# Performance work log

Hardware: AMD Instinct MI355X
Metric: run time of the kernel (lower is better)

The kernel has to match this reference:

```python
import jax, jax.numpy as jnp
import numpy as np

B, N, D, K, H, L = 4, 20000, 64, 256, 4, 2
F = 4 * D
DH = D // H
SCALE = DH ** -0.5
EPS = 1e-5


def _layernorm(x, g, b):
    m = jnp.mean(x, axis=-1, keepdims=True)
    v = jnp.mean(jnp.square(x - m), axis=-1, keepdims=True)
    return (x - m) / jnp.sqrt(v + EPS) * g + b


def setup_inputs() -> dict:
    key = jax.random.key(0)
    ks = jax.random.split(key, 12)
    s = 0.02
    return {
        'expr': jax.random.normal(ks[0], (B, N), jnp.float32),
        'emb': jax.random.normal(ks[1], (N, D), jnp.float32),
        'Wq': jax.random.normal(ks[2], (L, D, D), jnp.float32) * s,
        'Wk': jax.random.normal(ks[3], (L, D, D), jnp.float32) * s,
        'Wv': jax.random.normal(ks[4], (L, D, D), jnp.float32) * s,
        'projK': jax.random.normal(ks[5], (L, N, K), jnp.float32) * s,
        'projV': jax.random.normal(ks[6], (L, N, K), jnp.float32) * s,
        'Wo': jax.random.normal(ks[7], (L, D, D), jnp.float32) * s,
        'bo': jnp.zeros((L, D), jnp.float32),
        'g1': jnp.ones((L, D), jnp.float32),
        'be1': jnp.zeros((L, D), jnp.float32),
        'W1': jax.random.normal(ks[8], (L, D, F), jnp.float32) * s,
        'bf1': jnp.zeros((L, F), jnp.float32),
        'W2': jax.random.normal(ks[9], (L, F, D), jnp.float32) * s,
        'bf2': jnp.zeros((L, D), jnp.float32),
        'g2': jnp.ones((L, D), jnp.float32),
        'be2': jnp.zeros((L, D), jnp.float32),
    }


def _forward(expr, emb, Wq, Wk, Wv, projK, projV, Wo, bo, g1, be1, W1, bf1, W2, bf2, g2, be2):
    # gene_ids = arange(N) for every batch row -> embedding lookup is just the table
    x = emb[None, :, :] * expr[:, :, None]  # [B, N, D]
    for i in range(L):
        b = x.shape[0]
        # Linformer self-attention
        q = jnp.einsum('bnd,de->bne', x, Wq[i])                 # [B, N, D]
        k_low = jnp.einsum('bnd,nk->bkd', x, projK[i])          # [B, K, D]
        v_low = jnp.einsum('bnd,nk->bkd', x, projV[i])          # [B, K, D]
        k = jnp.einsum('bkd,de->bke', k_low, Wk[i])             # [B, K, D]
        v = jnp.einsum('bkd,de->bke', v_low, Wv[i])             # [B, K, D]
        qh = q.reshape(b, N, H, DH).transpose(0, 2, 1, 3)       # [B, H, N, DH]
        kh = k.reshape(b, K, H, DH).transpose(0, 2, 1, 3)       # [B, H, K, DH]
        vh = v.reshape(b, K, H, DH).transpose(0, 2, 1, 3)       # [B, H, K, DH]
        dots = jnp.einsum('bhnd,bhkd->bhnk', qh, kh) * SCALE    # [B, H, N, K]
        attn = jax.nn.softmax(dots, axis=-1)
        o = jnp.einsum('bhnk,bhkd->bhnd', attn, vh)             # [B, H, N, DH]
        o = o.transpose(0, 2, 1, 3).reshape(b, N, D)
        o = jnp.einsum('bnd,de->bne', o, Wo[i]) + bo[i]
        x = _layernorm(o + x, g1[i], be1[i])
        # FFN (exact GELU, matching torch nn.GELU default)
        h = jax.nn.gelu(jnp.einsum('bnd,df->bnf', x, W1[i]) + bf1[i], approximate=False)
        f = jnp.einsum('bnf,fd->bnd', h, W2[i]) + bf2[i]
        x = _layernorm(f + x, g2[i], be2[i])
    return x


def reference(expr, emb, Wq, Wk, Wv, projK, projV, Wo, bo, g1, be1, W1, bf1, W2, bf2, g2, be2):
    return _forward(expr, emb, Wq, Wk, Wv, projK, projV, Wo, bo, g1, be1, W1, bf1, W2, bf2, g2, be2)
```

## Files before the change

### kernel.cpp

```cpp
#include <hip/hip_runtime.h>

using u16 = unsigned short;
typedef __bf16 bf16x8 __attribute__((ext_vector_type(8)));
typedef u16    u16x8  __attribute__((ext_vector_type(8)));
typedef u16    u16x4  __attribute__((ext_vector_type(4)));
typedef float  f32x4  __attribute__((ext_vector_type(4)));
typedef float  f32x16 __attribute__((ext_vector_type(16)));
typedef unsigned uint4v __attribute__((ext_vector_type(4)));

#define DEV static __device__ __forceinline__

constexpr int NB = 4;
constexpr int NN = 20000;
constexpr int DD = 64;
constexpr int KK = 256;
constexpr int ROWS = NB * NN;

DEV float b2f(u16 u) { union { unsigned i; float f; } c; c.i = ((unsigned)u) << 16; return c.f; }
DEV u16 f2b(float f) {
  union { float f; unsigned i; } c; c.f = f;
  unsigned i = c.i + 0x7FFFu + ((c.i >> 16) & 1u);
  return (u16)(i >> 16);
}
DEV bf16x8 ldb8(const u16* p) { return *reinterpret_cast<const bf16x8*>(p); }
DEV f32x16 mfma32(bf16x8 a, bf16x8 b, f32x16 c) { return __builtin_amdgcn_mfma_f32_32x32x16_bf16(a, b, c, 0, 0, 0); }

DEV unsigned cvtpk(float lo, float hi) {
  unsigned r;
  asm("v_cvt_pk_bf16_f32 %0, %1, %2" : "=v"(r) : "v"(lo), "v"(hi));
  return r;
}
DEV void swap32(unsigned& a, unsigned& b) {
  auto r = __builtin_amdgcn_permlane32_swap((int)a, (int)b, false, false);
  a = (unsigned)r[0]; b = (unsigned)r[1];
}

__global__ __launch_bounds__(256) void k_pre(
    const float* __restrict__ expr, const float* __restrict__ emb,
    const float* __restrict__ Wq, const float* __restrict__ Wo,
    const float* __restrict__ W1, const float* __restrict__ W2,
    const float* __restrict__ projK, const float* __restrict__ projV,
    u16* __restrict__ wb, u16* __restrict__ pKT, u16* __restrict__ pVT,
    u16* __restrict__ xb, u16* __restrict__ ones) {
  __shared__ float lds[64][65];
  int bid = blockIdx.x;
  int t = threadIdx.x;
  if (bid < 5008) {
    int nt = bid % 313, q = bid / 313, kt = q & 3, z = q >> 2;
    int layer = z & 1, pv = z >> 1;
    const float* src = (pv ? projV : projK) + (size_t)layer * NN * KK;
    u16* dst = (pv ? pVT : pKT) + (size_t)layer * KK * NN;
    int n0 = nt * 64, k0 = kt * 64;
    int r = t >> 4, c4 = (t & 15) * 4;
#pragma unroll
    for (int i = 0; i < 4; ++i) {
      int rr = r + i * 16;
      float4 v = make_float4(0.f, 0.f, 0.f, 0.f);
      if (n0 + rr < NN) v = *reinterpret_cast<const float4*>(&src[(size_t)(n0 + rr) * KK + k0 + c4]);
      lds[c4 + 0][rr] = v.x; lds[c4 + 1][rr] = v.y; lds[c4 + 2][rr] = v.z; lds[c4 + 3][rr] = v.w;
    }
    __syncthreads();
    int kr = t >> 3, nb = (t & 7) * 8;
#pragma unroll
    for (int p = 0; p < 2; ++p) {
      int k = kr + p * 32;
      if (n0 + nb < NN) {
        u16x8 o;
#pragma unroll
        for (int j = 0; j < 8; ++j) o[j] = f2b(lds[k][nb + j]);
        *reinterpret_cast<u16x8*>(&dst[(size_t)(k0 + k) * NN + n0 + nb]) = o;
      }
    }
  } else if (bid < 7508) {
    int idx8 = ((bid - 5008) * 256 + t) * 8;
    int b = idx8 / (NN * DD);
    int rem = idx8 - b * (NN * DD);
    int n = rem >> 6, d = rem & 63;
    float4 e0 = *reinterpret_cast<const float4*>(&emb[(n << 6) + d]);
    float4 e1 = *reinterpret_cast<const float4*>(&emb[(n << 6) + d + 4]);
    float s = expr[b * NN + n];
    u16x8 o;
    o[0] = f2b(e0.x * s); o[1] = f2b(e0.y * s); o[2] = f2b(e0.z * s); o[3] = f2b(e0.w * s);
    o[4] = f2b(e1.x * s); o[5] = f2b(e1.y * s); o[6] = f2b(e1.z * s); o[7] = f2b(e1.w * s);
    *reinterpret_cast<u16x8*>(&xb[idx8]) = o;
  } else if (bid < 7572) {
    int b2 = bid - 7508;
    int bx = b2 & 7, m = (b2 >> 3) & 3, l = b2 >> 5;
    const float* src; u16* dst; int Dout, S, CT;
    if (m == 0)      { src = Wq + l * 4096;  dst = wb + l * 4096;          Dout = 64;  S = 4;  CT = 2; }
    else if (m == 1) { src = Wo + l * 4096;  dst = wb + 8192 + l * 4096;   Dout = 64;  S = 4;  CT = 2; }
    else if (m == 2) { src = W1 + l * 16384; dst = wb + 16384 + l * 16384; Dout = 256; S = 4;  CT = 8; }
    else             { src = W2 + l * 16384; dst = wb + 49152 + l * 16384; Dout = 64;  S = 16; CT = 2; }
    int slot = bx * 256 + t;
    if (slot >= S * CT * 64) return;
    int s = slot / (CT * 64), rem = slot % (CT * 64);
    int ct = rem >> 6, lane = rem & 63;
    int hi = lane >> 5, lo = lane & 31;
    u16x8 o;
#pragma unroll
    for (int j = 0; j < 8; ++j) o[j] = f2b(src[(s * 16 + hi * 8 + j) * Dout + ct * 32 + lo]);
    *reinterpret_cast<u16x8*>(&dst[slot * 8]) = o;
  } else {
    ones[t] = 0x3F80;
  }
}

__global__ __launch_bounds__(256) void k_qxt(
    const u16* __restrict__ x, const u16* __restrict__ WB,
    u16* __restrict__ qb, u16* __restrict__ xT) {
  __shared__ u16 ldsx[64][70];
  int bid = blockIdx.x;
  int t = threadIdx.x;
  if (bid < 625) {
    int w = t >> 6, lane = t & 63;
    int lo = lane & 31, hi = lane >> 5;
    int unit = bid * 4 + w;
    bf16x8 wf[4][2];
#pragma unroll
    for (int s = 0; s < 4; ++s)
#pragma unroll
      for (int ct = 0; ct < 2; ++ct) wf[s][ct] = ldb8(&WB[((s * 2 + ct) * 64 + lane) * 8]);
    f32x16 acc[2] = {};
    int r0 = unit * 32;
#pragma unroll
    for (int s = 0; s < 4; ++s) {
      bf16x8 a = ldb8(&x[(size_t)(r0 + lo) * 64 + s * 16 + hi * 8]);
      acc[0] = mfma32(a, wf[s][0], acc[0]);
      acc[1] = mfma32(a, wf[s][1], acc[1]);
    }
#pragma unroll
    for (int reg = 0; reg < 16; ++reg) {
      int row = r0 + (reg & 3) + 8 * (reg >> 2) + 4 * hi;
      qb[(size_t)row * 64 + lo] = f2b(acc[0][reg]);
      qb[(size_t)row * 64 + 32 + lo] = f2b(acc[1][reg]);
    }
  } else {
    int v = bid - 625;
    int nt = v % 313, b = v / 313;
    int n0 = nt * 64;
    int r = t >> 4, c4 = (t & 15) * 4;
    const u16* xbp = x + (size_t)b * NN * 64;
#pragma unroll
    for (int i = 0; i < 4; ++i) {
      int rr = r + i * 16;
      u16x4 vv = {};
      if (n0 + rr < NN) vv = *reinterpret_cast<const u16x4*>(&xbp[(size_t)(n0 + rr) * 64 + c4]);
      ldsx[c4 + 0][rr] = vv[0]; ldsx[c4 + 1][rr] = vv[1];
      ldsx[c4 + 2][rr] = vv[2]; ldsx[c4 + 3][rr] = vv[3];
    }
    __syncthreads();
    int dr = t >> 3, nb = (t & 7) * 8;
    u16* xo = xT + (size_t)b * 64 * NN;
#pragma unroll
    for (int p = 0; p < 2; ++p) {
      int d = dr + p * 32;
      if (n0 + nb < NN) {
        u16x8 o;
#pragma unroll
        for (int j = 0; j < 8; ++j) o[j] = ldsx[d][nb + j];
        *reinterpret_cast<u16x8*>(&xo[(size_t)d * NN + n0 + nb]) = o;
      }
    }
  }
}

__global__ __launch_bounds__(256) void k_proj(
    const u16* __restrict__ xT, const u16* __restrict__ pKT_l, const u16* __restrict__ pVT_l,
    float* __restrict__ part) {
  int c = blockIdx.x, b = blockIdx.y, proj = blockIdx.z;
  const u16* P = proj ? pVT_l : pKT_l;
  int t = threadIdx.x, w = t >> 6, lane = t & 63;
  int lo = lane & 31, hi = lane >> 5;
  int d0 = (w & 1) * 32;
  int kbase = (w >> 1) * 128;
  int n0 = c * 512;
  int rem = NN - n0;
  int steps = (rem < 512 ? rem : 512) >> 4;
  const u16* xr = xT + ((size_t)b * 64 + d0 + lo) * NN;
  f32x16 acc[4] = {};
  int s = 0;
  for (; s + 4 <= steps; s += 4) {
    bf16x8 a[4]; bf16x8 bv[4][4];
#pragma unroll
    for (int u = 0; u < 4; ++u) {
      int nb = n0 + (s + u) * 16 + hi * 8;
      a[u] = ldb8(&xr[nb]);
#pragma unroll
      for (int g = 0; g < 4; ++g) bv[u][g] = ldb8(&P[(size_t)(kbase + g * 32 + lo) * NN + nb]);
    }
#pragma unroll
    for (int u = 0; u < 4; ++u)
#pragma unroll
      for (int g = 0; g < 4; ++g) acc[g] = mfma32(a[u], bv[u][g], acc[g]);
  }
  for (; s < steps; ++s) {
    int nb = n0 + s * 16 + hi * 8;
    bf16x8 a = ldb8(&xr[nb]);
#pragma unroll
    for (int g = 0; g < 4; ++g) acc[g] = mfma32(a, ldb8(&P[(size_t)(kbase + g * 32 + lo) * NN + nb]), acc[g]);
  }
  float* dst = part + ((size_t)(proj * NB + b) * 40 + c) * (64 * 256);
#pragma unroll
  for (int g = 0; g < 4; ++g)
#pragma unroll
    for (int r = 0; r < 16; ++r) {
      int d = d0 + (r & 3) + 8 * (r >> 2) + 4 * hi;
      dst[d * 256 + kbase + g * 32 + lo] = acc[g][r];
    }
}

__global__ __launch_bounds__(256) void k_p2(
    const float* __restrict__ part, const float* __restrict__ Wk_l, const float* __restrict__ Wv_l,
    u16* __restrict__ kbuf, u16* __restrict__ vT) {
  int ks = blockIdx.x, b = blockIdx.y, proj = blockIdx.z;
  int k0 = ks * 8;
  const float* W = proj ? Wv_l : Wk_l;
  __shared__ float low[64][8];
  int t = threadIdx.x;
  const float* src = part + (size_t)(proj * NB + b) * 40 * (64 * 256);
#pragma unroll
  for (int i = 0; i < 2; ++i) {
    int idx = i * 256 + t;
    int e = idx >> 3, k = idx & 7;
    float s = 0.f;
    for (int cc = 0; cc < 40; ++cc) s += src[(size_t)cc * (64 * 256) + e * 256 + k0 + k];
    low[e][k] = s;
  }
  __syncthreads();
#pragma unroll
  for (int i = 0; i < 2; ++i) {
    int idx = i * 256 + t;
    int d = idx & 63, kk = idx >> 6;
    float a = 0.f;
#pragma unroll
    for (int e = 0; e < 64; ++e) a += low[e][kk] * W[e * 64 + d];
    if (proj == 0) {
      kbuf[((size_t)b * KK + k0 + kk) * 64 + d] = f2b(a * 0.3606737602222409f);
    } else {
      vT[((size_t)b * 64 + d) * KK + k0 + kk] = f2b(a);
    }
  }
}

__global__ __launch_bounds__(256) void k_attn(
    const u16* __restrict__ q, const u16* __restrict__ kbuf, const u16* __restrict__ vT,
    const u16* __restrict__ ones, u16* __restrict__ ao) {
  int t = threadIdx.x, h = t >> 6, lane = t & 63;
  int lo = lane & 31, hi = lane >> 5;
  int b = blockIdx.y;
  int n0 = blockIdx.x * 32;
  const u16* qb = q + (size_t)b * NN * 64;
  const u16* kb = kbuf + (size_t)b * KK * 64 + h * 16;
  const u16* vsrc = (lo < 16)
      ? vT + (size_t)b * 64 * KK + (size_t)(h * 16 + lo) * KK
      : ones;
  bf16x8 qf = ldb8(&qb[(size_t)(n0 + lo) * 64 + h * 16 + hi * 8]);
  f32x16 acc = {};
#pragma unroll
  for (int kt = 0; kt < 8; ++kt) {
    bf16x8 kf = ldb8(&kb[(size_t)(kt * 32 + lo) * 64 + hi * 8]);
    f32x16 z = {};
    f32x16 s = mfma32(kf, qf, z);
    float e[16];
#pragma unroll
    for (int r = 0; r < 16; ++r) e[r] = __builtin_amdgcn_exp2f(s[r]);
#pragma unroll
    for (int c = 0; c < 2; ++c) {
      unsigned Aw = cvtpk(e[c * 8 + 0], e[c * 8 + 1]);
      unsigned Bw = cvtpk(e[c * 8 + 2], e[c * 8 + 3]);
      unsigned Cw = cvtpk(e[c * 8 + 4], e[c * 8 + 5]);
      unsigned Dw = cvtpk(e[c * 8 + 6], e[c * 8 + 7]);
      swap32(Aw, Cw);
      swap32(Bw, Dw);
      uint4v pk; pk.x = Aw; pk.y = Bw; pk.z = Cw; pk.w = Dw;
      bf16x8 af = ldb8(&vsrc[kt * 32 + c * 16 + hi * 8]);
      acc = mfma32(af, __builtin_bit_cast(bf16x8, pk), acc);
    }
  }
  float inv = __builtin_amdgcn_rcpf(acc[8]);
  float o[8];
#pragma unroll
  for (int r = 0; r < 8; ++r) o[r] = acc[r] * inv;
  unsigned Aw = cvtpk(o[0], o[1]);
  unsigned Bw = cvtpk(o[2], o[3]);
  unsigned Cw = cvtpk(o[4], o[5]);
  unsigned Dw = cvtpk(o[6], o[7]);
  swap32(Aw, Cw);
  swap32(Bw, Dw);
  uint4v st; st.x = Aw; st.y = Bw; st.z = Cw; st.w = Dw;
  *reinterpret_cast<uint4v*>(&ao[(size_t)b * NN * 64 + (size_t)(n0 + lo) * 64 + h * 16 + hi * 8]) = st;
}

__global__ __launch_bounds__(256) void k_oln(
    const u16* __restrict__ A, const u16* __restrict__ WB,
    const float* __restrict__ bias, const u16* __restrict__ res,
    const float* __restrict__ g, const float* __restrict__ be, u16* __restrict__ out) {
  int t = threadIdx.x, w = t >> 6, lane = t & 63;
  int lo = lane & 31, hi = lane >> 5;
  int unit = blockIdx.x * 4 + w;
  bf16x8 wf[4][2];
#pragma unroll
  for (int s = 0; s < 4; ++s)
#pragma unroll
    for (int ct = 0; ct < 2; ++ct) wf[s][ct] = ldb8(&WB[((s * 2 + ct) * 64 + lane) * 8]);
  float bia[2], gg[2], bb[2];
#pragma unroll
  for (int ct = 0; ct < 2; ++ct) {
    bia[ct] = bias[ct * 32 + lo];
    gg[ct] = g[ct * 32 + lo];
    bb[ct] = be[ct * 32 + lo];
  }
  f32x16 acc[2] = {};
  int r0 = unit * 32;
#pragma unroll
  for (int s = 0; s < 4; ++s) {
    bf16x8 a = ldb8(&A[(size_t)(r0 + lo) * 64 + s * 16 + hi * 8]);
    acc[0] = mfma32(a, wf[s][0], acc[0]);
    acc[1] = mfma32(a, wf[s][1], acc[1]);
  }
#pragma unroll
  for (int reg = 0; reg < 16; ++reg) {
    int row = r0 + (reg & 3) + 8 * (reg >> 2) + 4 * hi;
    float a0 = acc[0][reg] + bia[0] + b2f(res[(size_t)row * 64 + lo]);
    float a1 = acc[1][reg] + bia[1] + b2f(res[(size_t)row * 64 + 32 + lo]);
    float su = a0 + a1, sq = a0 * a0 + a1 * a1;
#pragma unroll
    for (int m = 1; m <= 16; m <<= 1) { su += __shfl_xor(su, m); sq += __shfl_xor(sq, m); }
    float mean = su * (1.f / 64.f);
    float var = sq * (1.f / 64.f) - mean * mean;
    float rstd = rsqrtf(var + 1e-5f);
    out[(size_t)row * 64 + lo] = f2b((a0 - mean) * rstd * gg[0] + bb[0]);
    out[(size_t)row * 64 + 32 + lo] = f2b((a1 - mean) * rstd * gg[1] + bb[1]);
  }
}

__global__ __launch_bounds__(256, 2) void k_gemm_64_256(
    const u16* __restrict__ A, const u16* __restrict__ WB,
    const float* __restrict__ bias, u16* __restrict__ out) {
  int t = threadIdx.x, w = t >> 6, lane = t & 63;
  int lo = lane & 31, hi = lane >> 5;
  int colg = w & 1;
  int unit = blockIdx.x * 2 + (w >> 1);
  bf16x8 wf[4][4];
  float bia[4];
#pragma unroll
  for (int s = 0; s < 4; ++s)
#pragma unroll
    for (int ct = 0; ct < 4; ++ct) wf[s][ct] = ldb8(&WB[((s * 8 + colg * 4 + ct) * 64 + lane) * 8]);
#pragma unroll
  for (int ct = 0; ct < 4; ++ct) bia[ct] = bias[colg * 128 + ct * 32 + lo];
  f32x16 acc[4] = {};
  int r0 = unit * 32;
#pragma unroll
  for (int s = 0; s < 4; ++s) {
    bf16x8 a = ldb8(&A[(size_t)(r0 + lo) * 64 + s * 16 + hi * 8]);
#pragma unroll
    for (int ct = 0; ct < 4; ++ct) acc[ct] = mfma32(a, wf[s][ct], acc[ct]);
  }
#pragma unroll
  for (int ct = 0; ct < 4; ++ct) {
#pragma unroll
    for (int reg = 0; reg < 16; ++reg) {
      int row = r0 + (reg & 3) + 8 * (reg >> 2) + 4 * hi;
      float x = acc[ct][reg] + bia[ct];
      float gel = 0.5f * x * (1.f + erff(x * 0.7071067811865475f));
      out[(size_t)row * 256 + colg * 128 + ct * 32 + lo] = f2b(gel);
    }
  }
}

__global__ __launch_bounds__(256) void k_gemm_256_64(
    const u16* __restrict__ A, const u16* __restrict__ WB,
    const float* __restrict__ bias, const u16* __restrict__ res,
    const float* __restrict__ g, const float* __restrict__ be,
    u16* __restrict__ outb, float* __restrict__ outf) {
  int t = threadIdx.x, w = t >> 6, lane = t & 63;
  int lo = lane & 31, hi = lane >> 5;
  int unit = blockIdx.x * 4 + w;
  float bia[2], gg[2], bb[2];
#pragma unroll
  for (int ct = 0; ct < 2; ++ct) {
    bia[ct] = bias[ct * 32 + lo];
    gg[ct] = g[ct * 32 + lo];
    bb[ct] = be[ct * 32 + lo];
  }
  f32x16 acc[2] = {};
  int r0 = unit * 32;
#pragma unroll
  for (int s = 0; s < 16; ++s) {
    bf16x8 w0 = ldb8(&WB[((s * 2 + 0) * 64 + lane) * 8]);
    bf16x8 w1 = ldb8(&WB[((s * 2 + 1) * 64 + lane) * 8]);
    bf16x8 a = ldb8(&A[(size_t)(r0 + lo) * 256 + s * 16 + hi * 8]);
    acc[0] = mfma32(a, w0, acc[0]);
    acc[1] = mfma32(a, w1, acc[1]);
  }
#pragma unroll
  for (int reg = 0; reg < 16; ++reg) {
    int row = r0 + (reg & 3) + 8 * (reg >> 2) + 4 * hi;
    float a0 = acc[0][reg] + bia[0] + b2f(res[(size_t)row * 64 + lo]);
    float a1 = acc[1][reg] + bia[1] + b2f(res[(size_t)row * 64 + 32 + lo]);
    float su = a0 + a1, sq = a0 * a0 + a1 * a1;
#pragma unroll
    for (int m = 1; m <= 16; m <<= 1) { su += __shfl_xor(su, m); sq += __shfl_xor(sq, m); }
    float mean = su * (1.f / 64.f);
    float var = sq * (1.f / 64.f) - mean * mean;
    float rstd = rsqrtf(var + 1e-5f);
    float o0 = (a0 - mean) * rstd * gg[0] + bb[0];
    float o1 = (a1 - mean) * rstd * gg[1] + bb[1];
    if (outb) {
      outb[(size_t)row * 64 + lo] = f2b(o0);
      outb[(size_t)row * 64 + 32 + lo] = f2b(o1);
    }
    if (outf) {
      outf[(size_t)row * 64 + lo] = o0;
      outf[(size_t)row * 64 + 32 + lo] = o1;
    }
  }
}

extern "C" void kernel_launch(void* const* d_in, const int* in_sizes, int n_in,
                              void* d_out, int out_size, void* d_ws, size_t ws_size,
                              hipStream_t stream) {
  const float* expr = (const float*)d_in[0];
  const float* emb  = (const float*)d_in[1];
  const float* Wq   = (const float*)d_in[2];
  const float* Wk   = (const float*)d_in[3];
  const float* Wv   = (const float*)d_in[4];
  const float* projK = (const float*)d_in[5];
  const float* projV = (const float*)d_in[6];
  const float* Wo   = (const float*)d_in[7];
  const float* bo   = (const float*)d_in[8];
  const float* g1   = (const float*)d_in[9];
  const float* be1  = (const float*)d_in[10];
  const float* W1   = (const float*)d_in[11];
  const float* bf1  = (const float*)d_in[12];
  const float* W2   = (const float*)d_in[13];
  const float* bf2  = (const float*)d_in[14];
  const float* g2   = (const float*)d_in[15];
  const float* be2  = (const float*)d_in[16];
  float* out = (float*)d_out;
  char* ws = (char*)d_ws;

  u16* xb0 = (u16*)(ws + 0);
  u16* xb1 = (u16*)(ws + 10240000);
  u16* xb2 = (u16*)(ws + 20480000);
  u16* qb  = (u16*)(ws + 30720000);
  u16* aob = (u16*)(ws + 40960000);
  u16* hb  = (u16*)(ws + 51200000);
  float* part = (float*)(ws + 51200000);
  u16* pKT = (u16*)(ws + 92160000);
  u16* pVT = (u16*)(ws + 112640000);
  u16* xTb = (u16*)(ws + 133120000);
  u16* kB  = (u16*)(ws + 143360000);
  u16* vTB = (u16*)(ws + 143491072);
  u16* wb  = (u16*)(ws + 143622144);
  u16* ones = (u16*)(ws + 143785984);

  k_pre<<<7573, 256, 0, stream>>>(expr, emb, Wq, Wo, W1, W2, projK, projV,
                                  wb, pKT, pVT, xb0, ones);

  const u16* xin = xb0;
  for (int l = 0; l < 2; ++l) {
    const u16* wbq = wb + l * 4096;
    const u16* wbo = wb + 8192 + l * 4096;
    const u16* wb1 = wb + 16384 + l * 16384;
    const u16* wb2 = wb + 49152 + l * 16384;
    k_qxt<<<1877, 256, 0, stream>>>(xin, wbq, qb, xTb);
    k_proj<<<dim3(40, NB, 2), 256, 0, stream>>>(xTb, pKT + (size_t)l * KK * NN, pVT + (size_t)l * KK * NN, part);
    k_p2<<<dim3(32, NB, 2), 256, 0, stream>>>(part, Wk + l * 4096, Wv + l * 4096, kB, vTB);
    k_attn<<<dim3(625, NB), 256, 0, stream>>>(qb, kB, vTB, ones, aob);
    k_oln<<<625, 256, 0, stream>>>(aob, wbo, bo + l * 64, xin, g1 + l * 64, be1 + l * 64, xb1);
    k_gemm_64_256<<<1250, 256, 0, stream>>>(xb1, wb1, bf1 + l * 256, hb);
    k_gemm_256_64<<<625, 256, 0, stream>>>(hb, wb2, bf2 + l * 64, xb1,
                                           g2 + l * 64, be2 + l * 64,
                                           l == 0 ? xb2 : nullptr, l == 1 ? out : nullptr);
    xin = xb2;
  }
}
```

Measured before the change: 421.9 us.

## Fuse FFN up/down GEMMs with GELU in registers; widen projection transpose tiles

Merges the two FFN kernels into one. The GELU hidden activations stay in registers: they are repacked with permlane32 swaps into MFMA operand layout and fed straight into the second GEMM, with the residual add and layernorm folded into the epilogue. This removes the round-trip of the B×N×256 bf16 hidden tensor through global memory and one launch per layer. The preprocessing kernel also uses 128-row transpose tiles for the projection matrices, and the W1/W2 weight packing is changed to the transposed-operand layout the fused kernel expects. In exchange, each wave runs the whole FFN serially with more live registers, which may lower occupancy.

Result: faster. 405.1 us (-4.0%).

```diff
diff --git a/kernel.cpp b/kernel.cpp
--- a/kernel.cpp
+++ b/kernel.cpp
@@ -42,28 +42,35 @@
     const float* __restrict__ projK, const float* __restrict__ projV,
     u16* __restrict__ wb, u16* __restrict__ pKT, u16* __restrict__ pVT,
     u16* __restrict__ xb, u16* __restrict__ ones) {
-  __shared__ float lds[64][65];
+  __shared__ float lds[64][130];
   int bid = blockIdx.x;
   int t = threadIdx.x;
-  if (bid < 5008) {
-    int nt = bid % 313, q = bid / 313, kt = q & 3, z = q >> 2;
+  if (bid < 2512) {
+    int nt = bid % 157, q = bid / 157, kt = q & 3, z = q >> 2;
     int layer = z & 1, pv = z >> 1;
     const float* src = (pv ? projV : projK) + (size_t)layer * NN * KK;
     u16* dst = (pv ? pVT : pKT) + (size_t)layer * KK * NN;
-    int n0 = nt * 64, k0 = kt * 64;
-    int r = t >> 4, c4 = (t & 15) * 4;
-#pragma unroll
-    for (int i = 0; i < 4; ++i) {
-      int rr = r + i * 16;
-      float4 v = make_float4(0.f, 0.f, 0.f, 0.f);
-      if (n0 + rr < NN) v = *reinterpret_cast<const float4*>(&src[(size_t)(n0 + rr) * KK + k0 + c4]);
-      lds[c4 + 0][rr] = v.x; lds[c4 + 1][rr] = v.y; lds[c4 + 2][rr] = v.z; lds[c4 + 3][rr] = v.w;
+    int n0 = nt * 128, k0 = kt * 64;
+    int nr = t >> 1, kh = (t & 1) * 32;
+    float4 vv[8];
+    bool okr = (n0 + nr < NN);
+#pragma unroll
+    for (int q8 = 0; q8 < 8; ++q8) {
+      vv[q8] = make_float4(0.f, 0.f, 0.f, 0.f);
+      if (okr) vv[q8] = *reinterpret_cast<const float4*>(&src[(size_t)(n0 + nr) * KK + k0 + kh + q8 * 4]);
+    }
+#pragma unroll
+    for (int q8 = 0; q8 < 8; ++q8) {
+      lds[kh + q8 * 4 + 0][nr] = vv[q8].x;
+      lds[kh + q8 * 4 + 1][nr] = vv[q8].y;
+      lds[kh + q8 * 4 + 2][nr] = vv[q8].z;
+      lds[kh + q8 * 4 + 3][nr] = vv[q8].w;
     }
     __syncthreads();
-    int kr = t >> 3, nb = (t & 7) * 8;
-#pragma unroll
-    for (int p = 0; p < 2; ++p) {
-      int k = kr + p * 32;
+    int nb = (t & 15) * 8, kr = t >> 4;
+#pragma unroll
+    for (int p = 0; p < 4; ++p) {
+      int k = kr + p * 16;
       if (n0 + nb < NN) {
         u16x8 o;
 #pragma unroll
@@ -71,8 +78,8 @@
         *reinterpret_cast<u16x8*>(&dst[(size_t)(k0 + k) * NN + n0 + nb]) = o;
       }
     }
-  } else if (bid < 7508) {
-    int idx8 = ((bid - 5008) * 256 + t) * 8;
+  } else if (bid < 5012) {
+    int idx8 = ((bid - 2512) * 256 + t) * 8;
     int b = idx8 / (NN * DD);
     int rem = idx8 - b * (NN * DD);
     int n = rem >> 6, d = rem & 63;
@@ -83,23 +90,38 @@
     o[0] = f2b(e0.x * s); o[1] = f2b(e0.y * s); o[2] = f2b(e0.z * s); o[3] = f2b(e0.w * s);
     o[4] = f2b(e1.x * s); o[5] = f2b(e1.y * s); o[6] = f2b(e1.z * s); o[7] = f2b(e1.w * s);
     *reinterpret_cast<u16x8*>(&xb[idx8]) = o;
-  } else if (bid < 7572) {
-    int b2 = bid - 7508;
+  } else if (bid < 5076) {
+    int b2 = bid - 5012;
     int bx = b2 & 7, m = (b2 >> 3) & 3, l = b2 >> 5;
-    const float* src; u16* dst; int Dout, S, CT;
-    if (m == 0)      { src = Wq + l * 4096;  dst = wb + l * 4096;          Dout = 64;  S = 4;  CT = 2; }
-    else if (m == 1) { src = Wo + l * 4096;  dst = wb + 8192 + l * 4096;   Dout = 64;  S = 4;  CT = 2; }
-    else if (m == 2) { src = W1 + l * 16384; dst = wb + 16384 + l * 16384; Dout = 256; S = 4;  CT = 8; }
-    else             { src = W2 + l * 16384; dst = wb + 49152 + l * 16384; Dout = 64;  S = 16; CT = 2; }
     int slot = bx * 256 + t;
-    if (slot >= S * CT * 64) return;
-    int s = slot / (CT * 64), rem = slot % (CT * 64);
-    int ct = rem >> 6, lane = rem & 63;
-    int hi = lane >> 5, lo = lane & 31;
     u16x8 o;
-#pragma unroll
-    for (int j = 0; j < 8; ++j) o[j] = f2b(src[(s * 16 + hi * 8 + j) * Dout + ct * 32 + lo]);
-    *reinterpret_cast<u16x8*>(&dst[slot * 8]) = o;
+    if (m <= 1) {
+      if (slot >= 512) return;
+      int s = slot >> 7, rem = slot & 127;
+      int ct = rem >> 6, lane = rem & 63;
+      int hi = lane >> 5, lo = lane & 31;
+      const float* src = (m == 0 ? Wq : Wo) + l * 4096;
+      u16* dst = wb + (m == 0 ? 0 : 8192) + l * 4096;
+#pragma unroll
+      for (int j = 0; j < 8; ++j) o[j] = f2b(src[(s * 16 + hi * 8 + j) * 64 + ct * 32 + lo]);
+      *reinterpret_cast<u16x8*>(&dst[slot * 8]) = o;
+    } else if (m == 2) {
+      int ftile = slot >> 8, s = (slot >> 6) & 3, lane = slot & 63;
+      int hi = lane >> 5, lo = lane & 31;
+      const float* src = W1 + l * 16384;
+      u16* dst = wb + 16384 + l * 16384;
+#pragma unroll
+      for (int j = 0; j < 8; ++j) o[j] = f2b(src[(s * 16 + hi * 8 + j) * 256 + ftile * 32 + lo]);
+      *reinterpret_cast<u16x8*>(&dst[slot * 8]) = o;
+    } else {
+      int dtile = slot >> 10, s2 = (slot >> 6) & 15, lane = slot & 63;
+      int hi = lane >> 5, lo = lane & 31;
+      const float* src = W2 + l * 16384;
+      u16* dst = wb + 49152 + l * 16384;
+#pragma unroll
+      for (int j = 0; j < 8; ++j) o[j] = f2b(src[(s2 * 16 + hi * 8 + j) * 64 + dtile * 32 + lo]);
+      *reinterpret_cast<u16x8*>(&dst[slot * 8]) = o;
+    }
   } else {
     ones[t] = 0x3F80;
   }
@@ -334,86 +356,92 @@
   }
 }
 
-__global__ __launch_bounds__(256, 2) void k_gemm_64_256(
-    const u16* __restrict__ A, const u16* __restrict__ WB,
-    const float* __restrict__ bias, u16* __restrict__ out) {
-  int t = threadIdx.x, w = t >> 6, lane = t & 63;
-  int lo = lane & 31, hi = lane >> 5;
-  int colg = w & 1;
-  int unit = blockIdx.x * 2 + (w >> 1);
-  bf16x8 wf[4][4];
-  float bia[4];
-#pragma unroll
-  for (int s = 0; s < 4; ++s)
-#pragma unroll
-    for (int ct = 0; ct < 4; ++ct) wf[s][ct] = ldb8(&WB[((s * 8 + colg * 4 + ct) * 64 + lane) * 8]);
-#pragma unroll
-  for (int ct = 0; ct < 4; ++ct) bia[ct] = bias[colg * 128 + ct * 32 + lo];
-  f32x16 acc[4] = {};
-  int r0 = unit * 32;
-#pragma unroll
-  for (int s = 0; s < 4; ++s) {
-    bf16x8 a = ldb8(&A[(size_t)(r0 + lo) * 64 + s * 16 + hi * 8]);
-#pragma unroll
-    for (int ct = 0; ct < 4; ++ct) acc[ct] = mfma32(a, wf[s][ct], acc[ct]);
-  }
-#pragma unroll
-  for (int ct = 0; ct < 4; ++ct) {
-#pragma unroll
-    for (int reg = 0; reg < 16; ++reg) {
-      int row = r0 + (reg & 3) + 8 * (reg >> 2) + 4 * hi;
-      float x = acc[ct][reg] + bia[ct];
-      float gel = 0.5f * x * (1.f + erff(x * 0.7071067811865475f));
-      out[(size_t)row * 256 + colg * 128 + ct * 32 + lo] = f2b(gel);
-    }
-  }
-}
-
-__global__ __launch_bounds__(256) void k_gemm_256_64(
-    const u16* __restrict__ A, const u16* __restrict__ WB,
-    const float* __restrict__ bias, const u16* __restrict__ res,
+__global__ __launch_bounds__(256) void k_ffn(
+    const u16* __restrict__ A, const u16* __restrict__ W1T, const u16* __restrict__ W2T,
+    const float* __restrict__ b1, const float* __restrict__ b2,
     const float* __restrict__ g, const float* __restrict__ be,
     u16* __restrict__ outb, float* __restrict__ outf) {
   int t = threadIdx.x, w = t >> 6, lane = t & 63;
   int lo = lane & 31, hi = lane >> 5;
   int unit = blockIdx.x * 4 + w;
-  float bia[2], gg[2], bb[2];
-#pragma unroll
-  for (int ct = 0; ct < 2; ++ct) {
-    bia[ct] = bias[ct * 32 + lo];
-    gg[ct] = g[ct * 32 + lo];
-    bb[ct] = be[ct * 32 + lo];
-  }
-  f32x16 acc[2] = {};
   int r0 = unit * 32;
-#pragma unroll
-  for (int s = 0; s < 16; ++s) {
-    bf16x8 w0 = ldb8(&WB[((s * 2 + 0) * 64 + lane) * 8]);
-    bf16x8 w1 = ldb8(&WB[((s * 2 + 1) * 64 + lane) * 8]);
-    bf16x8 a = ldb8(&A[(size_t)(r0 + lo) * 256 + s * 16 + hi * 8]);
-    acc[0] = mfma32(a, w0, acc[0]);
-    acc[1] = mfma32(a, w1, acc[1]);
-  }
-#pragma unroll
-  for (int reg = 0; reg < 16; ++reg) {
-    int row = r0 + (reg & 3) + 8 * (reg >> 2) + 4 * hi;
-    float a0 = acc[0][reg] + bia[0] + b2f(res[(size_t)row * 64 + lo]);
-    float a1 = acc[1][reg] + bia[1] + b2f(res[(size_t)row * 64 + 32 + lo]);
-    float su = a0 + a1, sq = a0 * a0 + a1 * a1;
-#pragma unroll
-    for (int m = 1; m <= 16; m <<= 1) { su += __shfl_xor(su, m); sq += __shfl_xor(sq, m); }
-    float mean = su * (1.f / 64.f);
-    float var = sq * (1.f / 64.f) - mean * mean;
-    float rstd = rsqrtf(var + 1e-5f);
-    float o0 = (a0 - mean) * rstd * gg[0] + bb[0];
-    float o1 = (a1 - mean) * rstd * gg[1] + bb[1];
-    if (outb) {
-      outb[(size_t)row * 64 + lo] = f2b(o0);
-      outb[(size_t)row * 64 + 32 + lo] = f2b(o1);
-    }
-    if (outf) {
-      outf[(size_t)row * 64 + lo] = o0;
-      outf[(size_t)row * 64 + 32 + lo] = o1;
+  bf16x8 xf[4];
+#pragma unroll
+  for (int s = 0; s < 4; ++s) xf[s] = ldb8(&A[(size_t)(r0 + lo) * 64 + s * 16 + hi * 8]);
+  f32x16 oacc[2] = {};
+#pragma unroll
+  for (int ft = 0; ft < 8; ++ft) {
+    f32x16 hacc = {};
+#pragma unroll
+    for (int s = 0; s < 4; ++s)
+      hacc = mfma32(ldb8(&W1T[((ft * 4 + s) * 64 + lane) * 8]), xf[s], hacc);
+    float4 bb[4];
+#pragma unroll
+    for (int g4 = 0; g4 < 4; ++g4)
+      bb[g4] = *reinterpret_cast<const float4*>(&b1[ft * 32 + g4 * 8 + 4 * hi]);
+    float e[16];
+#pragma unroll
+    for (int r = 0; r < 16; ++r) {
+      float z = hacc[r] + bb[r >> 2][r & 3];
+      e[r] = 0.5f * z * (1.f + erff(z * 0.7071067811865475f));
+    }
+#pragma unroll
+    for (int c = 0; c < 2; ++c) {
+      unsigned Aw = cvtpk(e[c * 8 + 0], e[c * 8 + 1]);
+      unsigned Bw = cvtpk(e[c * 8 + 2], e[c * 8 + 3]);
+      unsigned Cw = cvtpk(e[c * 8 + 4], e[c * 8 + 5]);
+      unsigned Dw = cvtpk(e[c * 8 + 6], e[c * 8 + 7]);
+      swap32(Aw, Cw);
+      swap32(Bw, Dw);
+      uint4v pk; pk.x = Aw; pk.y = Bw; pk.z = Cw; pk.w = Dw;
+      bf16x8 pf = __builtin_bit_cast(bf16x8, pk);
+#pragma unroll
+      for (int dt = 0; dt < 2; ++dt)
+        oacc[dt] = mfma32(ldb8(&W2T[((dt * 16 + ft * 2 + c) * 64 + lane) * 8]), pf, oacc[dt]);
+    }
+  }
+  int n = r0 + lo;
+  float su = 0.f, sq = 0.f;
+#pragma unroll
+  for (int dt = 0; dt < 2; ++dt) {
+#pragma unroll
+    for (int m4 = 0; m4 < 4; ++m4) {
+      int d0 = dt * 32 + m4 * 8 + 4 * hi;
+      u16x4 rv = *reinterpret_cast<const u16x4*>(&A[(size_t)n * 64 + d0]);
+      float4 b2v = *reinterpret_cast<const float4*>(&b2[d0]);
+#pragma unroll
+      for (int j = 0; j < 4; ++j) {
+        int r = m4 * 4 + j;
+        float val = oacc[dt][r] + b2v[j] + b2f(rv[j]);
+        oacc[dt][r] = val;
+        su += val; sq += val * val;
+      }
+    }
+  }
+  su += __shfl_xor(su, 32);
+  sq += __shfl_xor(sq, 32);
+  float mean = su * (1.f / 64.f);
+  float var = sq * (1.f / 64.f) - mean * mean;
+  float rstd = rsqrtf(var + 1e-5f);
+#pragma unroll
+  for (int dt = 0; dt < 2; ++dt) {
+#pragma unroll
+    for (int m4 = 0; m4 < 4; ++m4) {
+      int d0 = dt * 32 + m4 * 8 + 4 * hi;
+      float4 gv = *reinterpret_cast<const float4*>(&g[d0]);
+      float4 bv = *reinterpret_cast<const float4*>(&be[d0]);
+      float q0 = (oacc[dt][m4 * 4 + 0] - mean) * rstd * gv.x + bv.x;
+      float q1 = (oacc[dt][m4 * 4 + 1] - mean) * rstd * gv.y + bv.y;
+      float q2 = (oacc[dt][m4 * 4 + 2] - mean) * rstd * gv.z + bv.z;
+      float q3 = (oacc[dt][m4 * 4 + 3] - mean) * rstd * gv.w + bv.w;
+      if (outb) {
+        unsigned w0 = cvtpk(q0, q1), w1 = cvtpk(q2, q3);
+        u16x4 st = __builtin_bit_cast(u16x4, make_uint2(w0, w1));
+        *reinterpret_cast<u16x4*>(&outb[(size_t)n * 64 + d0]) = st;
+      }
+      if (outf) {
+        *reinterpret_cast<float4*>(&outf[(size_t)n * 64 + d0]) = make_float4(q0, q1, q2, q3);
+      }
     }
   }
 }
@@ -446,7 +474,6 @@
   u16* xb2 = (u16*)(ws + 20480000);
   u16* qb  = (u16*)(ws + 30720000);
   u16* aob = (u16*)(ws + 40960000);
-  u16* hb  = (u16*)(ws + 51200000);
   float* part = (float*)(ws + 51200000);
   u16* pKT = (u16*)(ws + 92160000);
   u16* pVT = (u16*)(ws + 112640000);
@@ -456,7 +483,7 @@
   u16* wb  = (u16*)(ws + 143622144);
   u16* ones = (u16*)(ws + 143785984);
 
-  k_pre<<<7573, 256, 0, stream>>>(expr, emb, Wq, Wo, W1, W2, projK, projV,
+  k_pre<<<5077, 256, 0, stream>>>(expr, emb, Wq, Wo, W1, W2, projK, projV,
                                   wb, pKT, pVT, xb0, ones);
 
   const u16* xin = xb0;
@@ -470,10 +497,9 @@
     k_p2<<<dim3(32, NB, 2), 256, 0, stream>>>(part, Wk + l * 4096, Wv + l * 4096, kB, vTB);
     k_attn<<<dim3(625, NB), 256, 0, stream>>>(qb, kB, vTB, ones, aob);
     k_oln<<<625, 256, 0, stream>>>(aob, wbo, bo + l * 64, xin, g1 + l * 64, be1 + l * 64, xb1);
-    k_gemm_64_256<<<1250, 256, 0, stream>>>(xb1, wb1, bf1 + l * 256, hb);
-    k_gemm_256_64<<<625, 256, 0, stream>>>(hb, wb2, bf2 + l * 64, xb1,
-                                           g2 + l * 64, be2 + l * 64,
-                                           l == 0 ? xb2 : nullptr, l == 1 ? out : nullptr);
+    k_ffn<<<625, 256, 0, stream>>>(xb1, wb1, wb2, bf1 + l * 256, bf2 + l * 64,
+                                   g2 + l * 64, be2 + l * 64,
+                                   l == 0 ? xb2 : nullptr, l == 1 ? out : nullptr);
     xin = xb2;
   }
 }
```
